# Kernel tuning notes

Hardware: AMD Instinct MI355X
Metric: run time of the kernel (lower is better)

The kernel has to match this reference:

```python
import jax, jax.numpy as jnp
import numpy as np

N, L, S, D, H, DK = 4, 2048, 2048, 1024, 16, 64


def setup_inputs() -> dict:
    key = jax.random.key(0)
    kq, kk, kv, kwq, kwo = jax.random.split(key, 5)
    Q = jax.random.normal(kq, (N, L, D), dtype=jnp.float32)
    K = jax.random.normal(kk, (N, S, D), dtype=jnp.float32)
    V = jax.random.normal(kv, (N, S, D), dtype=jnp.float32)
    # per-head query projection weights (the source reuses Lq for K and V too)
    Wq = jax.random.normal(kwq, (H, DK, D), dtype=jnp.float32) * (D ** -0.5)
    # output projection Lo: Linear(h*dv -> Dv), weight shape (out, in)
    Wo = jax.random.normal(kwo, (D, H * DK), dtype=jnp.float32) * ((H * DK) ** -0.5)
    return {"Q": Q, "K": K, "V": V, "Wq": Wq, "Wo": Wo}


def reference(Q, K, V, Wq, Wo):
    dk = Wq.shape[1]
    # Faithful to source: ALL of q, k, v are projected with the Lq weights.
    q = jnp.einsum('nld,hkd->hnlk', Q, Wq)   # (H,N,L,dk)
    k = jnp.einsum('nsd,hkd->hnsk', K, Wq)   # (H,N,S,dk)
    v = jnp.einsum('nsd,hkd->hnsk', V, Wq)   # (H,N,S,dk)
    scale = jnp.asarray(dk, Q.dtype) ** 0.5
    scores = jnp.einsum('hnlk,hnsk->hnls', q, k) / scale  # (H,N,L,S)
    # Faithful to F.softmax(dot) with no dim on a 3D tensor: torch picks dim=0
    # (the batch axis N); here that is axis=1 of the head-stacked (H,N,L,S).
    attn = jax.nn.softmax(scores, axis=1)
    heads = jnp.einsum('hnls,hnsk->hnlk', attn, v)        # (H,N,L,dk)
    # concat heads along last dim -> (N,L,H*dk)
    heads = jnp.transpose(heads, (1, 2, 0, 3)).reshape(Q.shape[0], Q.shape[1], -1)
    return heads @ Wo.T  # (N,L,Dv)
```

## Files before the change

kernel.cpp:

```cpp
#include <hip/hip_runtime.h>
#include <hip/hip_bf16.h>

typedef __attribute__((ext_vector_type(8))) short short8;
typedef __attribute__((ext_vector_type(4))) short short4v;
typedef __attribute__((ext_vector_type(4))) float float4v;

#define DEVI static __device__ __forceinline__

#if __has_builtin(__builtin_amdgcn_exp2f)
#define EXP2(x) __builtin_amdgcn_exp2f(x)
#else
#define EXP2(x) exp2f(x)
#endif

DEVI unsigned short f2bf(float f) {
  unsigned int u = __builtin_bit_cast(unsigned int, f);
  u += 0x7fffu + ((u >> 16) & 1u);
  return (unsigned short)(u >> 16);
}

DEVI short8 pack8(float4v a, float4v b) {
  struct P4 { __hip_bfloat162 x, y, z, w; } t;
  t.x = __float22bfloat162_rn(make_float2(a[0], a[1]));
  t.y = __float22bfloat162_rn(make_float2(a[2], a[3]));
  t.z = __float22bfloat162_rn(make_float2(b[0], b[1]));
  t.w = __float22bfloat162_rn(make_float2(b[2], b[3]));
  short8 r;
  __builtin_memcpy(&r, &t, 16);
  return r;
}

DEVI short4v pack4(float a, float b, float c, float d) {
  struct P2 { __hip_bfloat162 x, y; } t;
  t.x = __float22bfloat162_rn(make_float2(a, b));
  t.y = __float22bfloat162_rn(make_float2(c, d));
  short4v r;
  __builtin_memcpy(&r, &t, 8);
  return r;
}

DEVI void gload16(const void* src, void* lds_dst) {
  __builtin_amdgcn_global_load_lds(
      (const __attribute__((address_space(1))) void*)src,
      (__attribute__((address_space(3))) void*)lds_dst, 16, 0, 0);
}

__global__ __launch_bounds__(256)
void cvt_bf16_2(const float* __restrict__ a, const float* __restrict__ b,
                unsigned short* __restrict__ oa, unsigned short* __restrict__ ob)
{
  int i = blockIdx.x * 256 + threadIdx.x;
  const float* src = (i < 131072) ? a : b;
  unsigned short* dst = (i < 131072) ? oa : ob;
  int j = (i < 131072) ? i : i - 131072;
  float4v x = *(const float4v*)(src + (size_t)j * 8);
  float4v y = *(const float4v*)(src + (size_t)j * 8 + 4);
  *(short8*)(dst + (size_t)j * 8) = pack8(x, y);
}

__global__ __launch_bounds__(256, 2)
void gemm_proj3(const float* __restrict__ Qp, const float* __restrict__ Kp,
                const float* __restrict__ Vp, const unsigned short* __restrict__ Bp,
                unsigned short* __restrict__ qb, unsigned short* __restrict__ kw,
                unsigned short* __restrict__ vt, float CS)
{
  constexpr int Kd = 1024, Nc = 1024, M = 8192;
  __shared__ alignas(16) short As[2][128 * 40];
  __shared__ alignas(16) short Bs[2][128 * 32];

  const int sel = blockIdx.y >> 3;
  const float* Af = (sel == 0) ? Qp : (sel == 1) ? Kp : Vp;
  unsigned short* Cp = (sel == 0) ? qb : (sel == 1) ? kw : vt;
  const float oscale = (sel == 0) ? CS : 1.0f;

  const int tid = threadIdx.x;
  const int lane = tid & 63;
  const int wid = tid >> 6;
  const int rl = lane & 15;
  const int g = lane >> 4;
  const int bm = blockIdx.x * 128;
  const int bn = (blockIdx.y & 7) * 128;
  const int wm = (wid >> 1) * 64;
  const int wn = (wid & 1) * 64;
  const int srow = tid >> 1;
  const int k0 = (tid & 1) * 16;

  float4v acc[4][4];
#pragma unroll
  for (int i = 0; i < 4; ++i)
#pragma unroll
    for (int j = 0; j < 4; ++j) acc[i][j] = (float4v)(0.0f);

  float4v afr[4];
  const int NK = Kd >> 5;
  const int grow = tid >> 2;
  const int gchk = tid & 3;

  auto stageB = [&](int ks, int b) {
#pragma unroll
    for (int j = 0; j < 2; ++j) {
      const unsigned short* src = Bp + (size_t)(bn + grow + j * 64) * Kd + ks * 32 + gchk * 8;
      gload16(src, (char*)Bs[b] + j * 4096 + wid * 1024);
    }
  };
  auto loadA = [&](int ks) {
    size_t base = (size_t)(bm + srow) * Kd + ks * 32 + k0;
    afr[0] = *(const float4v*)(Af + base);
    afr[1] = *(const float4v*)(Af + base + 4);
    afr[2] = *(const float4v*)(Af + base + 8);
    afr[3] = *(const float4v*)(Af + base + 12);
  };
  auto packWriteA = [&](int b) {
    *(short8*)(As[b] + srow * 40 + k0)     = pack8(afr[0], afr[1]);
    *(short8*)(As[b] + srow * 40 + k0 + 8) = pack8(afr[2], afr[3]);
  };

  stageB(0, 0);
  loadA(0);
  packWriteA(0);
  __syncthreads();

  for (int ks = 0; ks < NK; ++ks) {
    const int b = ks & 1;
    if (ks + 1 < NK) {
      stageB(ks + 1, b ^ 1);
      loadA(ks + 1);
    }

    short8 a8[4], b8[4];
#pragma unroll
    for (int mt = 0; mt < 4; ++mt)
      a8[mt] = *(const short8*)(As[b] + (wm + mt * 16 + rl) * 40 + 8 * g);
#pragma unroll
    for (int nt = 0; nt < 4; ++nt)
      b8[nt] = *(const short8*)(Bs[b] + (wn + nt * 16 + rl) * 32 + 8 * g);
#pragma unroll
    for (int mt = 0; mt < 4; ++mt)
#pragma unroll
      for (int nt = 0; nt < 4; ++nt)
        acc[mt][nt] = __builtin_amdgcn_mfma_f32_16x16x32_bf16(a8[mt], b8[nt], acc[mt][nt], 0, 0, 0);

    if (ks + 1 < NK) packWriteA(b ^ 1);
    __syncthreads();
  }

  if (sel != 2) {
#pragma unroll
    for (int mt = 0; mt < 4; ++mt)
#pragma unroll
      for (int nt = 0; nt < 4; ++nt) {
        const int col = bn + wn + nt * 16 + rl;
        const int row0 = bm + wm + mt * 16 + 4 * g;
#pragma unroll
        for (int r = 0; r < 4; ++r)
          Cp[(size_t)(row0 + r) * Nc + col] = f2bf(acc[mt][nt][r] * oscale);
      }
  } else {
#pragma unroll
    for (int mt = 0; mt < 4; ++mt)
#pragma unroll
      for (int nt = 0; nt < 4; ++nt) {
        const int col = bn + wn + nt * 16 + rl;
        const int row0 = bm + wm + mt * 16 + 4 * g;
        short4v w = pack4(acc[mt][nt][0], acc[mt][nt][1], acc[mt][nt][2], acc[mt][nt][3]);
        const int u = row0 & 31;
        const int pm = (row0 & ~31) | (((u >> 2) & 3) << 3) | (((u >> 4) & 1) << 2);
        *(short4v*)(Cp + (size_t)col * M + pm) = w;
      }
  }
}

__global__ __launch_bounds__(256, 2)
void gemm_out(const unsigned short* __restrict__ Ab, const unsigned short* __restrict__ Bp,
              float* __restrict__ Cp, int M, int Nc, int Kd)
{
  __shared__ alignas(16) short As[2][128 * 32];
  __shared__ alignas(16) short Bs[2][128 * 32];

  const int tid = threadIdx.x;
  const int lane = tid & 63;
  const int wid = tid >> 6;
  const int rl = lane & 15;
  const int g = lane >> 4;
  const int bm = blockIdx.x * 128;
  const int bn = blockIdx.y * 128;
  const int wm = (wid >> 1) * 64;
  const int wn = (wid & 1) * 64;

  float4v acc[4][4];
#pragma unroll
  for (int i = 0; i < 4; ++i)
#pragma unroll
    for (int j = 0; j < 4; ++j) acc[i][j] = (float4v)(0.0f);

  const int NK = Kd >> 5;
  const int grow = tid >> 2;
  const int gchk = tid & 3;

  auto stageAB = [&](int ks, int b) {
#pragma unroll
    for (int j = 0; j < 2; ++j) {
      const unsigned short* sa = Ab + (size_t)(bm + grow + j * 64) * Kd + ks * 32 + gchk * 8;
      gload16(sa, (char*)As[b] + j * 4096 + wid * 1024);
      const unsigned short* sb = Bp + (size_t)(bn + grow + j * 64) * Kd + ks * 32 + gchk * 8;
      gload16(sb, (char*)Bs[b] + j * 4096 + wid * 1024);
    }
  };

  stageAB(0, 0);
  __syncthreads();

  for (int ks = 0; ks < NK; ++ks) {
    const int b = ks & 1;
    if (ks + 1 < NK) stageAB(ks + 1, b ^ 1);

    short8 a8[4], b8[4];
#pragma unroll
    for (int mt = 0; mt < 4; ++mt)
      a8[mt] = *(const short8*)(As[b] + (wm + mt * 16 + rl) * 32 + 8 * g);
#pragma unroll
    for (int nt = 0; nt < 4; ++nt)
      b8[nt] = *(const short8*)(Bs[b] + (wn + nt * 16 + rl) * 32 + 8 * g);
#pragma unroll
    for (int mt = 0; mt < 4; ++mt)
#pragma unroll
      for (int nt = 0; nt < 4; ++nt)
        acc[mt][nt] = __builtin_amdgcn_mfma_f32_16x16x32_bf16(a8[mt], b8[nt], acc[mt][nt], 0, 0, 0);

    __syncthreads();
  }

#pragma unroll
  for (int mt = 0; mt < 4; ++mt)
#pragma unroll
    for (int nt = 0; nt < 4; ++nt) {
      const int col = bn + wn + nt * 16 + rl;
      const int row0 = bm + wm + mt * 16 + 4 * g;
#pragma unroll
      for (int r = 0; r < 4; ++r)
        Cp[(size_t)(row0 + r) * Nc + col] = acc[mt][nt][r];
    }
}

__global__ __launch_bounds__(512, 2)
void attn_bn(const unsigned short* __restrict__ qb,
             const unsigned short* __restrict__ kb,
             const unsigned short* __restrict__ vtb,
             unsigned short* __restrict__ hb)
{
  __shared__ alignas(128) char smem[131072];

  const int tid = threadIdx.x;
  const int lane = tid & 63;
  const int wid = tid >> 6;
  const int rl = lane & 15;
  const int g = lane >> 4;
  const int h = blockIdx.y;
  const int l0 = blockIdx.x * 128 + wid * 16;

  short8 qf[4][2];
#pragma unroll
  for (int n = 0; n < 4; ++n)
#pragma unroll
    for (int dh = 0; dh < 2; ++dh)
      qf[n][dh] = *(const short8*)(qb + (size_t)(n * 2048 + l0 + rl) * 1024 + h * 64 + dh * 32 + 8 * g);

  float4v ha[4][4];
#pragma unroll
  for (int n = 0; n < 4; ++n)
#pragma unroll
    for (int t = 0; t < 4; ++t) ha[n][t] = (float4v)(0.0f);

  const size_t koff0 = ((size_t)(wid * 2048) + (size_t)(lane >> 3)) * 1024
                     + (size_t)(h * 64) + (size_t)(((lane & 7) ^ (lane >> 3)) * 8);
  const size_t voff0 = ((size_t)(h * 64) + (size_t)(lane >> 2)) * 8192
                     + (size_t)((wid - 4) * 2048)
                     + (size_t)((((lane & 3) ^ ((lane >> 3) & 3)) * 8));

  auto stage = [&](int step, int b) {
    if (wid < 4) {
      char* kdst = smem + b * 32768 + wid * 4096;
      const unsigned short* ksrc = kb + koff0 + (size_t)step * 32 * 1024;
#pragma unroll
      for (int ii = 0; ii < 4; ++ii)
        gload16(ksrc + ii * 8192, kdst + ii * 1024);
    } else {
      char* vdst = smem + b * 32768 + 16384 + (wid - 4) * 4096;
      const unsigned short* vsrc = vtb + voff0 + (size_t)step * 32;
#pragma unroll
      for (int ii = 0; ii < 4; ++ii)
        gload16(vsrc + (size_t)ii * 16 * 8192, vdst + ii * 1024);
    }
  };

  stage(0, 0);
  stage(1, 1);
  stage(2, 2);
  asm volatile("s_waitcnt vmcnt(8)" ::: "memory");
  __builtin_amdgcn_s_barrier();

  const unsigned voffr = ((unsigned)(g ^ ((rl >> 1) & 3))) << 4;

  for (int to = 0; to < 16; ++to) {
#pragma unroll
    for (int ti = 0; ti < 4; ++ti) {
      const int t = to * 4 + ti;
      char* kbase = smem + ti * 32768;
      char* vbase = kbase + 16384;

      float4v sc[4][2];
      __builtin_amdgcn_s_setprio(1);
#pragma unroll
      for (int n = 0; n < 4; ++n) {
        char* kn = kbase + n * 4096;
#pragma unroll
        for (int ss = 0; ss < 2; ++ss) {
          const int srw = ss * 16 + rl;
          const unsigned sw = ((unsigned)(srw & 7)) << 4;
          short8 kf0 = *(const short8*)(kn + srw * 128 + ((16u * (unsigned)g) ^ sw));
          short8 kf1 = *(const short8*)(kn + srw * 128 + ((64u + 16u * (unsigned)g) ^ sw));
          float4v c = (float4v)(0.0f);
          c = __builtin_amdgcn_mfma_f32_16x16x32_bf16(kf0, qf[n][0], c, 0, 0, 0);
          c = __builtin_amdgcn_mfma_f32_16x16x32_bf16(kf1, qf[n][1], c, 0, 0, 0);
          sc[n][ss] = c;
        }
      }
      __builtin_amdgcn_s_setprio(0);

      float ex[4][2][4];
#pragma unroll
      for (int ss = 0; ss < 2; ++ss) {
#pragma unroll
        for (int n = 0; n < 4; ++n)
#pragma unroll
          for (int r = 0; r < 4; ++r)
            ex[n][ss][r] = EXP2(sc[n][ss][r]);
#pragma unroll
        for (int r = 0; r < 4; ++r) {
          float inv = __builtin_amdgcn_rcpf((ex[0][ss][r] + ex[1][ss][r])
                                          + (ex[2][ss][r] + ex[3][ss][r]) + 1e-30f);
          ex[0][ss][r] *= inv; ex[1][ss][r] *= inv;
          ex[2][ss][r] *= inv; ex[3][ss][r] *= inv;
        }
      }
      short8 pf8[4];
#pragma unroll
      for (int n = 0; n < 4; ++n) {
        float4v e0 = {ex[n][0][0], ex[n][0][1], ex[n][0][2], ex[n][0][3]};
        float4v e1 = {ex[n][1][0], ex[n][1][1], ex[n][1][2], ex[n][1][3]};
        pf8[n] = pack8(e0, e1);
      }

      __builtin_amdgcn_s_setprio(1);
#pragma unroll
      for (int n = 0; n < 4; ++n) {
        char* vn = vbase + n * 4096;
#pragma unroll
        for (int t4 = 0; t4 < 4; ++t4) {
          short8 va = *(const short8*)(vn + (t4 * 16 + rl) * 64 + voffr);
          ha[n][t4] = __builtin_amdgcn_mfma_f32_16x16x32_bf16(va, pf8[n], ha[n][t4], 0, 0, 0);
        }
      }
      __builtin_amdgcn_s_setprio(0);

      if (t + 3 < 64) stage(t + 3, (ti + 3) & 3);
      asm volatile("s_waitcnt vmcnt(8)" ::: "memory");
      __builtin_amdgcn_s_barrier();
    }
  }

#pragma unroll
  for (int n = 0; n < 4; ++n)
#pragma unroll
    for (int tt = 0; tt < 4; ++tt) {
      short4v w = pack4(ha[n][tt][0], ha[n][tt][1], ha[n][tt][2], ha[n][tt][3]);
      size_t off = (size_t)(n * 2048 + l0 + rl) * 1024 + h * 64 + tt * 16 + 4 * g;
      *(short4v*)(hb + off) = w;
    }
}

extern "C" void kernel_launch(void* const* d_in, const int* in_sizes, int n_in,
                              void* d_out, int out_size, void* d_ws, size_t ws_size,
                              hipStream_t stream)
{
  const float* Q  = (const float*)d_in[0];
  const float* K  = (const float*)d_in[1];
  const float* V  = (const float*)d_in[2];
  const float* Wq = (const float*)d_in[3];
  const float* Wo = (const float*)d_in[4];

  unsigned short* qb  = (unsigned short*)d_ws;
  unsigned short* kw  = qb + (size_t)8192 * 1024;
  unsigned short* vt  = kw + (size_t)8192 * 1024;
  unsigned short* wqb = vt + (size_t)8192 * 1024;
  unsigned short* wob = wqb + (size_t)1024 * 1024;
  unsigned short* hw  = qb;

  const float CS = 0.18033688011112042f;

  cvt_bf16_2<<<1024, 256, 0, stream>>>(Wq, Wo, wqb, wob);
  gemm_proj3<<<dim3(64, 24), dim3(256), 0, stream>>>(Q, K, V, wqb, qb, kw, vt, CS);
  attn_bn<<<dim3(16, 16), dim3(512), 0, stream>>>(qb, kw, vt, hw);
  gemm_out<<<dim3(64, 8), dim3(256), 0, stream>>>(hw, wob, (float*)d_out, 8192, 1024, 1024);
}
```

Measured before the change: 225.3 us.

## Software-pipeline QK scores one tile ahead of softmax and PV

Restructures the attention main loop so each iteration computes the QK MFMAs for the current tile while the exp/normalize and PV MFMAs consume the previous tile's scores. The goal is to overlap the exp/rcp VALU work with MFMA work and hide the score latency. The prologue stages a dummy buffer (slot 3) so the first PV iteration can run with a zero gate, and an epilogue finishes the last tile. The prefetch depth drops from three tiles to two, which may expose more global-load latency, and the extra score registers raise register pressure.

```diff
diff --git a/kernel.cpp b/kernel.cpp
--- a/kernel.cpp
+++ b/kernel.cpp
@@ -294,21 +294,30 @@
   };
 
   stage(0, 0);
+  stage(0, 3);
   stage(1, 1);
-  stage(2, 2);
-  asm volatile("s_waitcnt vmcnt(8)" ::: "memory");
+  asm volatile("s_waitcnt vmcnt(4)" ::: "memory");
   __builtin_amdgcn_s_barrier();
 
   const unsigned voffr = ((unsigned)(g ^ ((rl >> 1) & 3))) << 4;
+
+  float4v sc[2][4][2];
+#pragma unroll
+  for (int p = 0; p < 2; ++p)
+#pragma unroll
+    for (int n = 0; n < 4; ++n)
+#pragma unroll
+      for (int ss = 0; ss < 2; ++ss) sc[p][n][ss] = (float4v)(0.0f);
 
   for (int to = 0; to < 16; ++to) {
 #pragma unroll
     for (int ti = 0; ti < 4; ++ti) {
       const int t = to * 4 + ti;
+      const int cur = ti & 1;
+      const int prv = cur ^ 1;
       char* kbase = smem + ti * 32768;
-      char* vbase = kbase + 16384;
-
-      float4v sc[4][2];
+      char* vbase_prev = smem + (((ti + 3) & 3) * 32768) + 16384;
+
       __builtin_amdgcn_s_setprio(1);
 #pragma unroll
       for (int n = 0; n < 4; ++n) {
@@ -322,11 +331,11 @@
           float4v c = (float4v)(0.0f);
           c = __builtin_amdgcn_mfma_f32_16x16x32_bf16(kf0, qf[n][0], c, 0, 0, 0);
           c = __builtin_amdgcn_mfma_f32_16x16x32_bf16(kf1, qf[n][1], c, 0, 0, 0);
-          sc[n][ss] = c;
+          sc[cur][n][ss] = c;
         }
       }
-      __builtin_amdgcn_s_setprio(0);
-
+
+      const float gate = (to + ti == 0) ? 0.0f : 1.0f;
       float ex[4][2][4];
 #pragma unroll
       for (int ss = 0; ss < 2; ++ss) {
@@ -334,13 +343,14 @@
         for (int n = 0; n < 4; ++n)
 #pragma unroll
           for (int r = 0; r < 4; ++r)
-            ex[n][ss][r] = EXP2(sc[n][ss][r]);
+            ex[n][ss][r] = EXP2(sc[prv][n][ss][r]);
 #pragma unroll
         for (int r = 0; r < 4; ++r) {
           float inv = __builtin_amdgcn_rcpf((ex[0][ss][r] + ex[1][ss][r])
                                           + (ex[2][ss][r] + ex[3][ss][r]) + 1e-30f);
-          ex[0][ss][r] *= inv; ex[1][ss][r] *= inv;
-          ex[2][ss][r] *= inv; ex[3][ss][r] *= inv;
+          float ginv = inv * gate;
+          ex[0][ss][r] *= ginv; ex[1][ss][r] *= ginv;
+          ex[2][ss][r] *= ginv; ex[3][ss][r] *= ginv;
         }
       }
       short8 pf8[4];
@@ -351,10 +361,9 @@
         pf8[n] = pack8(e0, e1);
       }
 
-      __builtin_amdgcn_s_setprio(1);
 #pragma unroll
       for (int n = 0; n < 4; ++n) {
-        char* vn = vbase + n * 4096;
+        char* vn = vbase_prev + n * 4096;
 #pragma unroll
         for (int t4 = 0; t4 < 4; ++t4) {
           short8 va = *(const short8*)(vn + (t4 * 16 + rl) * 64 + voffr);
@@ -363,9 +372,45 @@
       }
       __builtin_amdgcn_s_setprio(0);
 
-      if (t + 3 < 64) stage(t + 3, (ti + 3) & 3);
-      asm volatile("s_waitcnt vmcnt(8)" ::: "memory");
+      if (t + 2 < 64) {
+        stage(t + 2, (ti + 2) & 3);
+        asm volatile("s_waitcnt vmcnt(4)" ::: "memory");
+      } else {
+        asm volatile("s_waitcnt vmcnt(0)" ::: "memory");
+      }
       __builtin_amdgcn_s_barrier();
+    }
+  }
+
+  {
+    float ex[4][2][4];
+#pragma unroll
+    for (int ss = 0; ss < 2; ++ss) {
+#pragma unroll
+      for (int n = 0; n < 4; ++n)
+#pragma unroll
+        for (int r = 0; r < 4; ++r)
+          ex[n][ss][r] = EXP2(sc[1][n][ss][r]);
+#pragma unroll
+      for (int r = 0; r < 4; ++r) {
+        float inv = __builtin_amdgcn_rcpf((ex[0][ss][r] + ex[1][ss][r])
+                                        + (ex[2][ss][r] + ex[3][ss][r]) + 1e-30f);
+        ex[0][ss][r] *= inv; ex[1][ss][r] *= inv;
+        ex[2][ss][r] *= inv; ex[3][ss][r] *= inv;
+      }
+    }
+    char* vbase = smem + 3 * 32768 + 16384;
+#pragma unroll
+    for (int n = 0; n < 4; ++n) {
+      float4v e0 = {ex[n][0][0], ex[n][0][1], ex[n][0][2], ex[n][0][3]};
+      float4v e1 = {ex[n][1][0], ex[n][1][1], ex[n][1][2], ex[n][1][3]};
+      short8 pf = pack8(e0, e1);
+      char* vn = vbase + n * 4096;
+#pragma unroll
+      for (int t4 = 0; t4 < 4; ++t4) {
+        short8 va = *(const short8*)(vn + (t4 * 16 + rl) * 64 + voffr);
+        ha[n][t4] = __builtin_amdgcn_mfma_f32_16x16x32_bf16(va, pf, ha[n][t4], 0, 0, 0);
+      }
     }
   }
 
```

After: 227.5 us. About the same (+1.0%).
